# Kernel optimization log

Measured on AMD Instinct MI355X. Metric: run time of the kernel, lower is better.

The kernel has to match this reference:

```python
import jax, jax.numpy as jnp
import numpy as np

# --- APPM / NMS pipeline constants (3 ratio groups on the 28x28 mixed feature map) ---
RATIOS = [4, 6, 8]            # square sliding-window sizes in feature cells
N_LIST = [2, 3, 2]            # proposals kept per group (proposalN = 7)
IOU_THRESHS = [0.25, 0.25, 0.25]
FM_SIZE = 28                  # mixed feature map spatial size
STRIDE = 16                   # 448 / 28: feature cell -> image pixels
IMG = 448
PROPOSAL_N = sum(N_LIST)
GROUP_SIZES = [(FM_SIZE - r + 1) ** 2 for r in RATIOS]


def make_coordinates():
    """[x0, y0, x1, y1] image-space boxes for every sliding window, all groups concatenated."""
    coords = []
    for r in RATIOS:
        n = FM_SIZE - r + 1
        ii, jj = np.meshgrid(np.arange(n), np.arange(n), indexing='ij')
        x0 = (ii.ravel() * STRIDE).astype(np.int32)
        y0 = (jj.ravel() * STRIDE).astype(np.int32)
        coords.append(np.stack([x0, y0, x0 + r * STRIDE, y0 + r * STRIDE], axis=1))
    return np.concatenate(coords, axis=0).astype(np.int32)   # (1595, 4)


def window_scores_from_fm(fm):
    """AvgPool2d(r, stride=1) then sum over channels == reduce_window over channel-summed map."""
    s = jnp.sum(fm, axis=1)  # (B, H, W)
    outs = []
    for r in RATIOS:
        w = jax.lax.reduce_window(s, 0.0, jax.lax.add, (1, r, r), (1, 1, 1), 'VALID') / float(r * r)
        outs.append(w.reshape(s.shape[0], -1))
    return jnp.concatenate(outs, axis=1)  # (B, sum(GROUP_SIZES))


def nms_group(scores, boxes, n_sel, thresh):
    """Greedy IoU NMS, exactly the inclusive (+1) box math of the source nms()."""
    areas = (boxes[:, 2] - boxes[:, 0] + 1.0) * (boxes[:, 3] - boxes[:, 1] + 1.0)

    def body(k, carry):
        sc, idxs = carry
        i = jnp.argmax(sc)                       # highest remaining score
        idxs = idxs.at[k].set(i.astype(jnp.int32))
        b = boxes[i]
        xx0 = jnp.maximum(boxes[:, 0], b[0]); yy0 = jnp.maximum(boxes[:, 1], b[1])
        xx1 = jnp.minimum(boxes[:, 2], b[2]); yy1 = jnp.minimum(boxes[:, 3], b[3])
        w = xx1 - xx0 + 1.0; h = yy1 - yy0 + 1.0
        inter = jnp.where((w < 0) | (h < 0), 0.0, w * h)
        iou = inter / (areas + areas[i] - inter)
        sc = jnp.where(iou > thresh, -jnp.inf, sc)  # suppress (selected box has iou=1 -> removed)
        return sc, idxs

    _, idxs = jax.lax.fori_loop(0, n_sel, body, (scores, jnp.zeros((n_sel,), jnp.int32)))
    return idxs


def select_proposals(all_scores, coordinates):
    parts = []
    off = 0
    for ng, n_sel, th in zip(GROUP_SIZES, N_LIST, IOU_THRESHS):
        sc = all_scores[:, off:off + ng]
        bx = coordinates[off:off + ng].astype(jnp.float32)
        idx = jax.vmap(lambda s: nms_group(s, bx, n_sel, th))(sc) + off
        parts.append(idx)
        off += ng
    return jnp.concatenate(parts, axis=1)  # (B, PROPOSAL_N) global window indices


def crop_windows(x, coordinates, indices):
    """Gather-crop each proposal window from the raw image, bilinear-resize to 448x448."""
    outs = []
    col = 0
    for r, n_sel in zip(RATIOS, N_LIST):
        w = r * STRIDE  # fixed crop size for this ratio group
        idx_g = indices[:, col:col + n_sel]

        def crop_one(img, gi):
            c = coordinates[gi]
            patch = jax.lax.dynamic_slice(img, (0, c[0], c[1]), (3, w, w))
            return jax.image.resize(patch, (3, IMG, IMG), 'bilinear')

        crops = jax.vmap(lambda img, gis: jax.vmap(lambda gi: crop_one(img, gi))(gis))(x, idx_g)
        outs.append(crops)
        col += n_sel
    return jnp.concatenate(outs, axis=1)  # (B, PROPOSAL_N, 3, 448, 448)


def setup_inputs() -> dict:
    key = jax.random.key(0)
    k1, k2, k3, k4 = jax.random.split(key, 4)
    B = 8
    return {
        'x': jax.random.normal(k1, (B, 3, IMG, IMG), jnp.float32),
        'fm': jax.random.normal(k2, (B, 384, FM_SIZE, FM_SIZE), jnp.float32),
        'embedding': jax.random.normal(k3, (B, 2048), jnp.float32),
        'W_cls': jax.random.normal(k4, (2048, 200), jnp.float32) * 0.02,
        'b_cls': jnp.zeros((200,), jnp.float32),
        'coordinates': jnp.asarray(make_coordinates()),
    }


def reference(x, fm, embedding, W_cls, b_cls, coordinates):
    all_scores = window_scores_from_fm(fm)                              # window_scores (B, 1595)
    proposalN_indices = select_proposals(all_scores, coordinates)       # (B, 7) int32
    proposalN_windows_scores = jnp.take_along_axis(all_scores, proposalN_indices, axis=1)
    window_imgs = crop_windows(x, coordinates, proposalN_indices)
    window_imgs = window_imgs.reshape(-1, 3, IMG, IMG)                  # (B*7, 3, 448, 448)
    raw_logits = embedding @ W_cls + b_cls                              # rawcls_net
    return (proposalN_indices, proposalN_windows_scores, all_scores, window_imgs, raw_logits)
```

## Files before the change

kernel.cpp:

```cpp
#include <hip/hip_runtime.h>
#include <math.h>

#define THREADS 256
#define CROP_GRID 1024
#define NTASK (56 * 3 * 28)

typedef float f32x4 __attribute__((ext_vector_type(4)));

template <int LK>
__global__ __launch_bounds__(THREADS) void fused1_kernel(const float* __restrict__ fm,
                                                         float4* __restrict__ part,
                                                         int cpc, int K,
                                                         const float* __restrict__ emb,
                                                         const float* __restrict__ W,
                                                         float* __restrict__ lpart) {
    constexpr int LROWS = 2048 / LK;
    int blk = blockIdx.x;
    int t = threadIdx.x;
    if (blk < 8 * K) {
        int b = blk / K, k = blk - b * K;
        if (t >= 196) return;
        const float4* f = (const float4*)(fm + ((size_t)b * 384 + (size_t)k * cpc) * 784);
        float4 acc = {0.0f, 0.0f, 0.0f, 0.0f};
        for (int c = 0; c < cpc; ++c) {
            float4 v = f[(size_t)c * 196 + t];
            acc.x += v.x; acc.y += v.y; acc.z += v.z; acc.w += v.w;
        }
        part[((size_t)b * K + k) * 196 + t] = acc;
    } else {
        int idx = blk - 8 * K;
        int b = idx / LK, kc = idx - b * LK;
        if (t >= 200) return;
        const float* e  = emb + (size_t)b * 2048 + kc * LROWS;
        const float* wp = W + (size_t)kc * LROWS * 200 + t;
        float a0 = 0.0f, a1 = 0.0f, a2 = 0.0f, a3 = 0.0f;
        #pragma unroll
        for (int k = 0; k < LROWS; k += 4) {
            a0 += e[k]     * wp[(size_t)k * 200];
            a1 += e[k + 1] * wp[(size_t)(k + 1) * 200];
            a2 += e[k + 2] * wp[(size_t)(k + 2) * 200];
            a3 += e[k + 3] * wp[(size_t)(k + 3) * 200];
        }
        lpart[((size_t)b * LK + kc) * 200 + t] = (a0 + a1) + (a2 + a3);
    }
}

template <int LK>
__global__ __launch_bounds__(THREADS) void fused2_kernel(const float4* __restrict__ part,
                                                         int K,
                                                         float* __restrict__ all_scores,
                                                         float* __restrict__ out_idx_f,
                                                         float* __restrict__ out_sc,
                                                         int* __restrict__ ws_idx,
                                                         int* __restrict__ soff,
                                                         const int* __restrict__ coords,
                                                         const float* __restrict__ lpart,
                                                         const float* __restrict__ bias,
                                                         float* __restrict__ logits) {
    __shared__ float4 s4[196];
    __shared__ float  pref[28][29];
    __shared__ float  scl[625];
    __shared__ float  rv[4];
    __shared__ int    ri[4];
    int t = threadIdx.x;

    if (blockIdx.x >= 24) {
        int b = blockIdx.x - 24;
        if (t >= 200) return;
        float a0 = bias[t], a1 = 0.0f, a2 = 0.0f, a3 = 0.0f;
        const float* lp = lpart + (size_t)b * LK * 200 + t;
        #pragma unroll
        for (int kc = 0; kc < LK; kc += 4) {
            a0 += lp[(size_t)kc * 200];
            a1 += lp[(size_t)(kc + 1) * 200];
            a2 += lp[(size_t)(kc + 2) * 200];
            a3 += lp[(size_t)(kc + 3) * 200];
        }
        logits[b * 200 + t] = (a0 + a1) + (a2 + a3);
        return;
    }

    int b = blockIdx.x / 3, g = blockIdx.x - b * 3;

    if (t < 196) {
        float4 acc = {0.0f, 0.0f, 0.0f, 0.0f};
        #pragma unroll 16
        for (int k = 0; k < K; ++k) {
            float4 v = part[((size_t)b * K + k) * 196 + t];
            acc.x += v.x; acc.y += v.y; acc.z += v.z; acc.w += v.w;
        }
        s4[t] = acc;
    }
    __syncthreads();
    if (t < 28) {
        float4 row[7];
        #pragma unroll
        for (int i = 0; i < 7; ++i) row[i] = s4[t * 7 + i];
        float run = 0.0f;
        pref[t][0] = 0.0f;
        #pragma unroll
        for (int j = 0; j < 28; ++j) {
            run += ((float*)row)[j];
            pref[t][j + 1] = run;
        }
    }
    __syncthreads();

    const int gnA[3]   = {625, 529, 441};
    const int sideA[3] = {25, 23, 21};
    const int rA[3]    = {4, 6, 8};
    const int nselA[3] = {2, 3, 2};
    const int colA[3]  = {0, 2, 5};
    const int goffA[3] = {0, 625, 1154};

    int n = gnA[g], side = sideA[g], r = rA[g];
    int nsel = nselA[g], goff = goffA[g], colbase = colA[g];
    float inv = 1.0f / (float)(r * r);

    for (int loc = t; loc < n; loc += THREADS) {
        int i = loc / side, j = loc % side;
        float acc = 0.0f;
        for (int a = 0; a < r; ++a)
            acc += pref[i + a][j + r] - pref[i + a][j];
        float sv = acc * inv;
        scl[loc] = sv;
        all_scores[b * 1595 + goff + loc] = sv;
    }
    __syncthreads();

    float ext = (float)(r * 16 + 1);
    float A   = ext * ext;
    float rs  = (float)(r * 16);

    for (int k = 0; k < nsel; ++k) {
        float bv = -INFINITY; int bi = 0x7fffffff;
        for (int i = t; i < n; i += THREADS) {
            float v = scl[i];
            if (v > bv || (v == bv && i < bi)) { bv = v; bi = i; }
        }
        #pragma unroll
        for (int m = 1; m < 64; m <<= 1) {
            float ov = __shfl_xor(bv, m, 64);
            int   oi = __shfl_xor(bi, m, 64);
            if (ov > bv || (ov == bv && oi < bi)) { bv = ov; bi = oi; }
        }
        int wv = t >> 6;
        if ((t & 63) == 0) { rv[wv] = bv; ri[wv] = bi; }
        __syncthreads();
        if (t == 0) {
            for (int q = 1; q < 4; ++q) {
                float ov = rv[q]; int oi = ri[q];
                if (ov > bv || (ov == bv && oi < bi)) { bv = ov; bi = oi; }
            }
            ri[0] = bi;
            int outp = b * 7 + colbase + k;
            int gi   = goff + bi;
            out_idx_f[outp] = (float)gi;
            out_sc[outp]    = bv;
            ws_idx[outp]    = gi;
            soff[outp]      = coords[gi * 4 + 0] * 448 + coords[gi * 4 + 1];
        }
        __syncthreads();
        int sel = ri[0];
        int si = sel / side, sj = sel % side;
        float sx0 = si * 16.0f, sy0 = sj * 16.0f;
        float sx1 = sx0 + rs,   sy1 = sy0 + rs;
        for (int i = t; i < n; i += THREADS) {
            int ii = i / side, jj = i % side;
            float x0 = ii * 16.0f, y0 = jj * 16.0f;
            float x1 = x0 + rs,    y1 = y0 + rs;
            float xx0 = fmaxf(x0, sx0), yy0 = fmaxf(y0, sy0);
            float xx1 = fminf(x1, sx1), yy1 = fminf(y1, sy1);
            float w = xx1 - xx0 + 1.0f, h = yy1 - yy0 + 1.0f;
            float inter = (w < 0.0f || h < 0.0f) ? 0.0f : w * h;
            float iou = inter / (A + A - inter);
            if (iou > 0.25f) scl[i] = -INFINITY;
        }
        __syncthreads();
    }
}

__global__ __launch_bounds__(448) void crop_kernel(const float* __restrict__ x,
                                                   const int* __restrict__ soff,
                                                   float* __restrict__ out) {
    __shared__ float lds[2][924];
    int t = threadIdx.x;

    int rr0 = t / 132, xx0 = t - rr0 * 132;
    int i1  = t + 448;
    int rr1 = i1 / 132, xx1 = i1 - rr1 * 132;
    int xx2 = t + 104;
    int row_sub = t / 56;
    int seg     = t - row_sub * 56;
    int ox0 = seg * 8;

    int task = blockIdx.x;
    int cw; float cscale, cwm1; int cS, crlo; float* coutb;
    float rA, rB, rC = 0.0f;
    {
        int p = task / 84, rem = task - p * 84;
        int ch = rem / 28, stripe = rem - ch * 28;
        int b = p / 7, col = p - b * 7;
        int g = (col < 2) ? 0 : ((col < 5) ? 1 : 2);
        cw = (g == 0) ? 64 : ((g == 1) ? 96 : 128);
        cscale = (float)cw * (1.0f / 448.0f);
        cwm1 = (float)(cw - 1);
        cS = stripe * 16;
        float syb = fminf(fmaxf(((float)cS + 0.5f) * cscale - 0.5f, 0.0f), cwm1);
        crlo = (int)syb;
        const float* cbase = x + ((size_t)(b * 3 + ch)) * 200704 + soff[p];
        coutb = out + ((size_t)(p * 3 + ch)) * 200704;
        rA = cbase[(size_t)min(crlo + rr0, cw - 1) * 448 + min(xx0, cw - 1)];
        rB = cbase[(size_t)min(crlo + rr1, cw - 1) * 448 + min(xx1, cw - 1)];
        if (t < 28)
            rC = cbase[(size_t)min(crlo + 6, cw - 1) * 448 + min(xx2, cw - 1)];
    }

    int buf = 0;
    while (true) {
        int nxt = task + CROP_GRID;
        bool has = nxt < NTASK;

        lds[buf][t]       = rA;
        lds[buf][t + 448] = rB;
        if (t < 28) lds[buf][t + 896] = rC;

        int nw = 0, nrlo = 0, nS = 0;
        float nscale = 0.0f, nwm1 = 0.0f;
        float* noutb = nullptr;
        if (has) {
            int p = nxt / 84, rem = nxt - p * 84;
            int ch = rem / 28, stripe = rem - ch * 28;
            int b = p / 7, col = p - b * 7;
            int g = (col < 2) ? 0 : ((col < 5) ? 1 : 2);
            nw = (g == 0) ? 64 : ((g == 1) ? 96 : 128);
            nscale = (float)nw * (1.0f / 448.0f);
            nwm1 = (float)(nw - 1);
            nS = stripe * 16;
            float syb = fminf(fmaxf(((float)nS + 0.5f) * nscale - 0.5f, 0.0f), nwm1);
            nrlo = (int)syb;
            const float* nbase = x + ((size_t)(b * 3 + ch)) * 200704 + soff[p];
            noutb = out + ((size_t)(p * 3 + ch)) * 200704;
            rA = nbase[(size_t)min(nrlo + rr0, nw - 1) * 448 + min(xx0, nw - 1)];
            rB = nbase[(size_t)min(nrlo + rr1, nw - 1) * 448 + min(xx1, nw - 1)];
            if (t < 28)
                rC = nbase[(size_t)min(nrlo + 6, nw - 1) * 448 + min(xx2, nw - 1)];
        }

        __syncthreads();

        {
            float sxb = ((float)ox0 + 0.5f) * cscale - 0.5f;
            float sxc = fminf(fmaxf(sxb, 0.0f), cwm1);
            int   i0  = (int)sxc;
            float txk[8];
            bool  e1[8], e2[8];
            #pragma unroll
            for (int k = 0; k < 8; ++k) {
                float sx = fminf(fmaxf(sxb + (float)k * cscale, 0.0f), cwm1);
                int xi = (int)sx;
                txk[k] = sx - (float)xi;
                int d  = xi - i0;
                e1[k] = (d >= 1);
                e2[k] = (d >= 2);
            }
            const float* lbase = &lds[buf][0];
            #pragma unroll
            for (int half = 0; half < 2; ++half) {
                int oy = cS + half * 8 + row_sub;
                float sy = fminf(fmaxf(((float)oy + 0.5f) * cscale - 0.5f, 0.0f), cwm1);
                int   y0 = (int)sy;
                int   y1 = min(y0 + 1, cw - 1);
                float ty = sy - (float)y0;
                const float* l0 = lbase + (y0 - crlo) * 132 + i0;
                const float* l1 = lbase + (y1 - crlo) * 132 + i0;
                float a0 = l0[0], a1 = l0[1], a2 = l0[2], a3 = l0[3];
                float b0 = l1[0], b1 = l1[1], b2 = l1[2], b3 = l1[3];
                float da0 = a1 - a0, da1 = a2 - a1, da2 = a3 - a2;
                float db0 = b1 - b0, db1 = b2 - b1, db2 = b3 - b2;

                f32x4 res0, res1;
                #pragma unroll
                for (int k = 0; k < 8; ++k) {
                    float av  = e2[k] ? a2  : (e1[k] ? a1  : a0);
                    float dav = e2[k] ? da2 : (e1[k] ? da1 : da0);
                    float bv  = e2[k] ? b2  : (e1[k] ? b1  : b0);
                    float dbv = e2[k] ? db2 : (e1[k] ? db1 : db0);
                    float top = fmaf(txk[k], dav, av);
                    float bot = fmaf(txk[k], dbv, bv);
                    float rr  = top + ty * (bot - top);
                    if (k < 4) res0[k] = rr; else res1[k - 4] = rr;
                }
                float* orow = coutb + (size_t)oy * 448 + ox0;
                *(f32x4*)orow       = res0;
                *(f32x4*)(orow + 4) = res1;
            }
        }

        if (!has) break;
        cw = nw; cscale = nscale; cwm1 = nwm1; cS = nS; crlo = nrlo; coutb = noutb;
        task = nxt;
        buf ^= 1;
    }
}

extern "C" void kernel_launch(void* const* d_in, const int* in_sizes, int n_in,
                              void* d_out, int out_size, void* d_ws, size_t ws_size,
                              hipStream_t stream) {
    const float* x      = (const float*)d_in[0];
    const float* fm     = (const float*)d_in[1];
    const float* emb    = (const float*)d_in[2];
    const float* Wc     = (const float*)d_in[3];
    const float* bc     = (const float*)d_in[4];
    const int*   coords = (const int*)d_in[5];

    float* out        = (float*)d_out;
    float* out_idx    = out;
    float* out_sc     = out + 56;
    float* all_scores = out + 112;
    float* imgs       = out + 12872;
    float* logits     = out + 33731144;

    int K = 32;
    while (K > 1 && ws_size < 1024 + (size_t)8 * K * 784 * 4 + (size_t)8 * 64 * 200 * 4)
        K >>= 1;
    int cpc = 384 / K;

    int*    ws_idx = (int*)d_ws;
    int*    soff   = (int*)((char*)d_ws + 256);
    float4* part   = (float4*)((char*)d_ws + 1024);
    float*  lpart  = (float*)((char*)d_ws + 1024 + (size_t)8 * K * 784 * 4);

    fused1_kernel<64><<<8 * K + 8 * 64, THREADS, 0, stream>>>(fm, part, cpc, K, emb, Wc, lpart);
    fused2_kernel<64><<<32, THREADS, 0, stream>>>(part, K, all_scores, out_idx, out_sc, ws_idx,
                                                  soff, coords, lpart, bc, logits);
    crop_kernel<<<CROP_GRID, 448, 0, stream>>>(x, soff, imgs);
}
```

Baseline: 48.39 us.

## Merge reduction and NMS kernels into one launch with atomic completion counters

```diff
diff --git a/kernel.cpp b/kernel.cpp
--- a/kernel.cpp
+++ b/kernel.cpp
@@ -4,89 +4,111 @@
 #define THREADS 256
 #define CROP_GRID 1024
 #define NTASK (56 * 3 * 28)
+#define CS_K 32
+#define LG_K 64
 
 typedef float f32x4 __attribute__((ext_vector_type(4)));
 
-template <int LK>
-__global__ __launch_bounds__(THREADS) void fused1_kernel(const float* __restrict__ fm,
+__global__ __launch_bounds__(THREADS) void stage1_kernel(const float* __restrict__ fm,
                                                          float4* __restrict__ part,
-                                                         int cpc, int K,
                                                          const float* __restrict__ emb,
                                                          const float* __restrict__ W,
-                                                         float* __restrict__ lpart) {
-    constexpr int LROWS = 2048 / LK;
-    int blk = blockIdx.x;
-    int t = threadIdx.x;
-    if (blk < 8 * K) {
-        int b = blk / K, k = blk - b * K;
-        if (t >= 196) return;
-        const float4* f = (const float4*)(fm + ((size_t)b * 384 + (size_t)k * cpc) * 784);
-        float4 acc = {0.0f, 0.0f, 0.0f, 0.0f};
-        for (int c = 0; c < cpc; ++c) {
-            float4 v = f[(size_t)c * 196 + t];
-            acc.x += v.x; acc.y += v.y; acc.z += v.z; acc.w += v.w;
-        }
-        part[((size_t)b * K + k) * 196 + t] = acc;
-    } else {
-        int idx = blk - 8 * K;
-        int b = idx / LK, kc = idx - b * LK;
-        if (t >= 200) return;
-        const float* e  = emb + (size_t)b * 2048 + kc * LROWS;
-        const float* wp = W + (size_t)kc * LROWS * 200 + t;
-        float a0 = 0.0f, a1 = 0.0f, a2 = 0.0f, a3 = 0.0f;
-        #pragma unroll
-        for (int k = 0; k < LROWS; k += 4) {
-            a0 += e[k]     * wp[(size_t)k * 200];
-            a1 += e[k + 1] * wp[(size_t)(k + 1) * 200];
-            a2 += e[k + 2] * wp[(size_t)(k + 2) * 200];
-            a3 += e[k + 3] * wp[(size_t)(k + 3) * 200];
-        }
-        lpart[((size_t)b * LK + kc) * 200 + t] = (a0 + a1) + (a2 + a3);
-    }
-}
-
-template <int LK>
-__global__ __launch_bounds__(THREADS) void fused2_kernel(const float4* __restrict__ part,
-                                                         int K,
+                                                         float* __restrict__ lpart,
+                                                         const int* __restrict__ coords,
                                                          float* __restrict__ all_scores,
                                                          float* __restrict__ out_idx_f,
                                                          float* __restrict__ out_sc,
                                                          int* __restrict__ ws_idx,
                                                          int* __restrict__ soff,
-                                                         const int* __restrict__ coords,
-                                                         const float* __restrict__ lpart,
                                                          const float* __restrict__ bias,
-                                                         float* __restrict__ logits) {
+                                                         float* __restrict__ logits,
+                                                         int* __restrict__ done) {
+    int blk = blockIdx.x;
+    int t = threadIdx.x;
+
+    if (blk < 256) {
+        int b = blk >> 5, k = blk & 31;
+        if (t < 196) {
+            const float4* f = (const float4*)(fm + ((size_t)b * 384 + (size_t)k * 12) * 784);
+            float4 acc = {0.0f, 0.0f, 0.0f, 0.0f};
+            #pragma unroll
+            for (int c = 0; c < 12; ++c) {
+                float4 v = f[(size_t)c * 196 + t];
+                acc.x += v.x; acc.y += v.y; acc.z += v.z; acc.w += v.w;
+            }
+            part[((size_t)b * CS_K + k) * 196 + t] = acc;
+        }
+        __syncthreads();
+        if (t == 0)
+            __hip_atomic_fetch_add(&done[b], 1, __ATOMIC_RELEASE, __HIP_MEMORY_SCOPE_AGENT);
+        return;
+    }
+
+    if (blk < 768) {
+        int idx = blk - 256;
+        int b = idx >> 6, kc = idx & 63;
+        if (t < 200) {
+            const float* e  = emb + (size_t)b * 2048 + kc * 32;
+            const float* wp = W + (size_t)kc * 32 * 200 + t;
+            float a0 = 0.0f, a1 = 0.0f, a2 = 0.0f, a3 = 0.0f;
+            #pragma unroll
+            for (int k = 0; k < 32; k += 4) {
+                a0 += e[k]     * wp[(size_t)k * 200];
+                a1 += e[k + 1] * wp[(size_t)(k + 1) * 200];
+                a2 += e[k + 2] * wp[(size_t)(k + 2) * 200];
+                a3 += e[k + 3] * wp[(size_t)(k + 3) * 200];
+            }
+            lpart[((size_t)b * LG_K + kc) * 200 + t] = (a0 + a1) + (a2 + a3);
+        }
+        __syncthreads();
+        if (t == 0)
+            __hip_atomic_fetch_add(&done[8 + b], 1, __ATOMIC_RELEASE, __HIP_MEMORY_SCOPE_AGENT);
+        return;
+    }
+
+    if (blk >= 792) {
+        int b = blk - 792;
+        if (t == 0) {
+            while (__hip_atomic_load(&done[8 + b], __ATOMIC_ACQUIRE,
+                                     __HIP_MEMORY_SCOPE_AGENT) < 64)
+                __builtin_amdgcn_s_sleep(2);
+        }
+        __syncthreads();
+        if (t >= 200) return;
+        float a0 = bias[t], a1 = 0.0f, a2 = 0.0f, a3 = 0.0f;
+        const float* lp = lpart + (size_t)b * LG_K * 200 + t;
+        #pragma unroll
+        for (int kc = 0; kc < LG_K; kc += 4) {
+            a0 += lp[(size_t)kc * 200];
+            a1 += lp[(size_t)(kc + 1) * 200];
+            a2 += lp[(size_t)(kc + 2) * 200];
+            a3 += lp[(size_t)(kc + 3) * 200];
+        }
+        logits[b * 200 + t] = (a0 + a1) + (a2 + a3);
+        return;
+    }
+
     __shared__ float4 s4[196];
     __shared__ float  pref[28][29];
     __shared__ float  scl[625];
     __shared__ float  rv[4];
     __shared__ int    ri[4];
-    int t = threadIdx.x;
-
-    if (blockIdx.x >= 24) {
-        int b = blockIdx.x - 24;
-        if (t >= 200) return;
-        float a0 = bias[t], a1 = 0.0f, a2 = 0.0f, a3 = 0.0f;
-        const float* lp = lpart + (size_t)b * LK * 200 + t;
-        #pragma unroll
-        for (int kc = 0; kc < LK; kc += 4) {
-            a0 += lp[(size_t)kc * 200];
-            a1 += lp[(size_t)(kc + 1) * 200];
-            a2 += lp[(size_t)(kc + 2) * 200];
-            a3 += lp[(size_t)(kc + 3) * 200];
-        }
-        logits[b * 200 + t] = (a0 + a1) + (a2 + a3);
-        return;
-    }
-
-    int b = blockIdx.x / 3, g = blockIdx.x - b * 3;
+
+    int i = blk - 768;
+    int b = i / 3, g = i - b * 3;
+
+    if (t == 0) {
+        while (__hip_atomic_load(&done[b], __ATOMIC_ACQUIRE,
+                                 __HIP_MEMORY_SCOPE_AGENT) < CS_K)
+            __builtin_amdgcn_s_sleep(2);
+    }
+    __syncthreads();
 
     if (t < 196) {
         float4 acc = {0.0f, 0.0f, 0.0f, 0.0f};
         #pragma unroll 16
-        for (int k = 0; k < K; ++k) {
-            float4 v = part[((size_t)b * K + k) * 196 + t];
+        for (int k = 0; k < CS_K; ++k) {
+            float4 v = part[((size_t)b * CS_K + k) * 196 + t];
             acc.x += v.x; acc.y += v.y; acc.z += v.z; acc.w += v.w;
         }
         s4[t] = acc;
@@ -95,7 +117,7 @@
     if (t < 28) {
         float4 row[7];
         #pragma unroll
-        for (int i = 0; i < 7; ++i) row[i] = s4[t * 7 + i];
+        for (int q = 0; q < 7; ++q) row[q] = s4[t * 7 + q];
         float run = 0.0f;
         pref[t][0] = 0.0f;
         #pragma unroll
@@ -118,10 +140,10 @@
     float inv = 1.0f / (float)(r * r);
 
     for (int loc = t; loc < n; loc += THREADS) {
-        int i = loc / side, j = loc % side;
+        int ii = loc / side, j = loc % side;
         float acc = 0.0f;
         for (int a = 0; a < r; ++a)
-            acc += pref[i + a][j + r] - pref[i + a][j];
+            acc += pref[ii + a][j + r] - pref[ii + a][j];
         float sv = acc * inv;
         scl[loc] = sv;
         all_scores[b * 1595 + goff + loc] = sv;
@@ -134,9 +156,9 @@
 
     for (int k = 0; k < nsel; ++k) {
         float bv = -INFINITY; int bi = 0x7fffffff;
-        for (int i = t; i < n; i += THREADS) {
-            float v = scl[i];
-            if (v > bv || (v == bv && i < bi)) { bv = v; bi = i; }
+        for (int q = t; q < n; q += THREADS) {
+            float v = scl[q];
+            if (v > bv || (v == bv && q < bi)) { bv = v; bi = q; }
         }
         #pragma unroll
         for (int m = 1; m < 64; m <<= 1) {
@@ -165,8 +187,8 @@
         int si = sel / side, sj = sel % side;
         float sx0 = si * 16.0f, sy0 = sj * 16.0f;
         float sx1 = sx0 + rs,   sy1 = sy0 + rs;
-        for (int i = t; i < n; i += THREADS) {
-            int ii = i / side, jj = i % side;
+        for (int q = t; q < n; q += THREADS) {
+            int ii = q / side, jj = q % side;
             float x0 = ii * 16.0f, y0 = jj * 16.0f;
             float x1 = x0 + rs,    y1 = y0 + rs;
             float xx0 = fmaxf(x0, sx0), yy0 = fmaxf(y0, sy0);
@@ -174,7 +196,7 @@
             float w = xx1 - xx0 + 1.0f, h = yy1 - yy0 + 1.0f;
             float inter = (w < 0.0f || h < 0.0f) ? 0.0f : w * h;
             float iou = inter / (A + A - inter);
-            if (iou > 0.25f) scl[i] = -INFINITY;
+            if (iou > 0.25f) scl[q] = -INFINITY;
         }
         __syncthreads();
     }
@@ -321,18 +343,15 @@
     float* imgs       = out + 12872;
     float* logits     = out + 33731144;
 
-    int K = 32;
-    while (K > 1 && ws_size < 1024 + (size_t)8 * K * 784 * 4 + (size_t)8 * 64 * 200 * 4)
-        K >>= 1;
-    int cpc = 384 / K;
-
     int*    ws_idx = (int*)d_ws;
     int*    soff   = (int*)((char*)d_ws + 256);
+    int*    done   = (int*)((char*)d_ws + 512);
     float4* part   = (float4*)((char*)d_ws + 1024);
-    float*  lpart  = (float*)((char*)d_ws + 1024 + (size_t)8 * K * 784 * 4);
-
-    fused1_kernel<64><<<8 * K + 8 * 64, THREADS, 0, stream>>>(fm, part, cpc, K, emb, Wc, lpart);
-    fused2_kernel<64><<<32, THREADS, 0, stream>>>(part, K, all_scores, out_idx, out_sc, ws_idx,
-                                                  soff, coords, lpart, bc, logits);
+    float*  lpart  = (float*)((char*)d_ws + 1024 + (size_t)8 * CS_K * 784 * 4);
+
+    hipMemsetAsync(done, 0, 64, stream);
+    stage1_kernel<<<800, THREADS, 0, stream>>>(fm, part, emb, Wc, lpart, coords,
+                                               all_scores, out_idx, out_sc, ws_idx,
+                                               soff, bc, logits, done);
     crop_kernel<<<CROP_GRID, 448, 0, stream>>>(x, soff, imgs);
 }
```

After: 72.96 us. +50.8%, slower.

## Run greedy NMS in a single wavefront with register-resident scores

Applied to the files above, without the earlier changes.

```diff
diff --git a/kernel.cpp b/kernel.cpp
--- a/kernel.cpp
+++ b/kernel.cpp
@@ -60,8 +60,6 @@
     __shared__ float4 s4[196];
     __shared__ float  pref[28][29];
     __shared__ float  scl[625];
-    __shared__ float  rv[4];
-    __shared__ int    ri[4];
     int t = threadIdx.x;
 
     if (blockIdx.x >= 24) {
@@ -128,15 +126,24 @@
     }
     __syncthreads();
 
+    if (t >= 64) return;
+
+    int PER = (n + 63) / 64;
+    int base = t * PER;
+    float val[10];
+    #pragma unroll
+    for (int q = 0; q < 10; ++q)
+        val[q] = (q < PER && base + q < n) ? scl[base + q] : -INFINITY;
+
     float ext = (float)(r * 16 + 1);
     float A   = ext * ext;
     float rs  = (float)(r * 16);
 
     for (int k = 0; k < nsel; ++k) {
         float bv = -INFINITY; int bi = 0x7fffffff;
-        for (int i = t; i < n; i += THREADS) {
-            float v = scl[i];
-            if (v > bv || (v == bv && i < bi)) { bv = v; bi = i; }
+        #pragma unroll
+        for (int q = 0; q < 10; ++q) {
+            if (q < PER && val[q] > bv) { bv = val[q]; bi = base + q; }
         }
         #pragma unroll
         for (int m = 1; m < 64; m <<= 1) {
@@ -144,15 +151,7 @@
             int   oi = __shfl_xor(bi, m, 64);
             if (ov > bv || (ov == bv && oi < bi)) { bv = ov; bi = oi; }
         }
-        int wv = t >> 6;
-        if ((t & 63) == 0) { rv[wv] = bv; ri[wv] = bi; }
-        __syncthreads();
         if (t == 0) {
-            for (int q = 1; q < 4; ++q) {
-                float ov = rv[q]; int oi = ri[q];
-                if (ov > bv || (ov == bv && oi < bi)) { bv = ov; bi = oi; }
-            }
-            ri[0] = bi;
             int outp = b * 7 + colbase + k;
             int gi   = goff + bi;
             out_idx_f[outp] = (float)gi;
@@ -160,13 +159,15 @@
             ws_idx[outp]    = gi;
             soff[outp]      = coords[gi * 4 + 0] * 448 + coords[gi * 4 + 1];
         }
-        __syncthreads();
-        int sel = ri[0];
-        int si = sel / side, sj = sel % side;
+        int si = bi / side, sj = bi % side;
         float sx0 = si * 16.0f, sy0 = sj * 16.0f;
         float sx1 = sx0 + rs,   sy1 = sy0 + rs;
-        for (int i = t; i < n; i += THREADS) {
-            int ii = i / side, jj = i % side;
+        #pragma unroll
+        for (int q = 0; q < 10; ++q) {
+            if (q >= PER) continue;
+            int idx = base + q;
+            if (idx >= n) continue;
+            int ii = idx / side, jj = idx % side;
             float x0 = ii * 16.0f, y0 = jj * 16.0f;
             float x1 = x0 + rs,    y1 = y0 + rs;
             float xx0 = fmaxf(x0, sx0), yy0 = fmaxf(y0, sy0);
@@ -174,9 +175,8 @@
             float w = xx1 - xx0 + 1.0f, h = yy1 - yy0 + 1.0f;
             float inter = (w < 0.0f || h < 0.0f) ? 0.0f : w * h;
             float iou = inter / (A + A - inter);
-            if (iou > 0.25f) scl[i] = -INFINITY;
-        }
-        __syncthreads();
+            if (iou > 0.25f) val[q] = -INFINITY;
+        }
     }
 }
 
```

Measured after the change: 48.60 us. No clear change (+0.4%).
